# Kernel tuning notes

Measured on AMD Instinct MI355X. Metric: run time of the kernel, lower is better.

## Reference

```python
import jax, jax.numpy as jnp
import numpy as np

TOP_K = 2

def setup_inputs() -> dict:
    key = jax.random.key(0)
    ks = jax.random.split(key, 5)
    B, S, D, E, R, H = 4, 2048, 1024, 8, 128, 4096
    s = 0.02
    return {
        "hidden_states": jax.random.normal(ks[0], (B, S, D), jnp.float32),
        "w_route": jax.random.normal(ks[1], (E, D, R), jnp.float32) * s,
        "w3": jax.random.normal(ks[2], (E, D, H), jnp.float32) * s,
        "wr2h": jax.random.normal(ks[3], (E, R, H), jnp.float32) * s,
        "wh2d": jax.random.normal(ks[4], (E, H, D), jnp.float32) * s,
    }

def reference(hidden_states, w_route, w3, wr2h, wh2d):
    B, S, D = hidden_states.shape
    E = w_route.shape[0]
    x = hidden_states.reshape(-1, D)                      # [N, D]
    N = x.shape[0]
    # per-expert routing activations (also reused as w1_state inside experts)
    acts = jnp.einsum('nd,edr->ner', x, w_route)          # [N, E, R]
    norms = jnp.linalg.norm(acts, axis=-1)                # [N, E] router logits
    probs = jax.nn.softmax(norms.astype(jnp.float32), axis=-1)
    topw, sel = jax.lax.top_k(probs, TOP_K)               # [N, k]
    topw = topw / topw.sum(axis=-1, keepdims=True)
    topw = topw.astype(x.dtype)
    # dense combine weights: routing weight if expert selected, else 0
    combine = jnp.zeros((N, E), x.dtype).at[jnp.arange(N)[:, None], sel].add(topw)
    out = jnp.zeros_like(x)
    for e in range(E):  # fixed small expert count
        h = (x @ w3[e]) * jax.nn.silu(acts[:, e, :] @ wr2h[e])  # [N, H]
        out = out + (h @ wh2d[e]) * combine[:, e:e + 1]
    final = out.reshape(B, S, D)
    # load balancing loss on the router logits (expert_act_norms)
    mask = jax.nn.one_hot(sel, E, dtype=jnp.float32)      # [N, k, E]
    tokens_per_expert = mask.mean(axis=0)                 # [k, E]
    router_prob_per_expert = probs.mean(axis=0)           # [E]
    bl_loss = jnp.sum(tokens_per_expert * router_prob_per_expert[None, :]) * E
    return final, norms, bl_loss
```

## Files before the change

kernel.cpp:

```cpp
#include <hip/hip_runtime.h>


#define DEV static __device__ __forceinline__

typedef float  f32x4  __attribute__((ext_vector_type(4)));
typedef __bf16 bf16x8 __attribute__((ext_vector_type(8)));

#define VMCNT_(n) asm volatile("s_waitcnt vmcnt(" #n ")" ::: "memory")
#define VMCNT(n) VMCNT_(n)

DEV unsigned short f2bf(float f) {
  union { float f; unsigned u; } v; v.f = f;
  unsigned r = v.u + 0x7fffu + ((v.u >> 16) & 1u);
  return (unsigned short)(r >> 16);
}
DEV float bf2f(unsigned short b) {
  union { unsigned u; float f; } v; v.u = ((unsigned)b) << 16;
  return v.f;
}

DEV void gll16(const void* g, void* l) {
  __builtin_amdgcn_global_load_lds(
      (const __attribute__((address_space(1))) unsigned int*)g,
      (__attribute__((address_space(3))) unsigned int*)l, 16, 0, 0);
}

DEV f32x4 mfma16(bf16x8 a, bf16x8 b, f32x4 c) {
  return __builtin_amdgcn_mfma_f32_16x16x32_bf16(a, b, c, 0, 0, 0);
}

DEV int xcd_swz_gen(int bid, int nwg) {
  int x = bid & 7, o = bid >> 3;
  int q = nwg >> 3, r = nwg & 7;
  return (x < r ? x * (q + 1) : r * (q + 1) + (x - r) * q) + o;
}

DEV bf16x8 frag_read(const unsigned short* lds, int row, int kb) {
  int off = row * 128 + ((kb * 2) ^ ((row & 7) << 4));
  return *(const bf16x8*)((const char*)lds + off);
}
DEV void stage_linear(const unsigned short* base, size_t pitch, int k0,
                      unsigned short* lds, int tid) {
  int wq = tid >> 6, lane = tid & 63;
#pragma unroll
  for (int i = 0; i < 4; ++i) {
    int s = wq * 256 + i * 64 + lane;
    int row = s >> 3, b = s & 7;
    int bb = b ^ (row & 7);
    const unsigned short* g = base + (size_t)row * pitch + (size_t)(k0 + bb * 8);
    gll16(g, lds + (size_t)(wq * 256 + i * 64) * 8);
  }
}
DEV void stage_gather(const unsigned short* base, size_t pitch, size_t colOff,
                      int k0, const int* toks, unsigned short* lds, int tid) {
  int wq = tid >> 6, lane = tid & 63;
#pragma unroll
  for (int i = 0; i < 4; ++i) {
    int s = wq * 256 + i * 64 + lane;
    int row = s >> 3, b = s & 7;
    int bb = b ^ (row & 7);
    const unsigned short* g =
        base + (size_t)toks[row] * pitch + colOff + (size_t)(k0 + bb * 8);
    gll16(g, lds + (size_t)(wq * 256 + i * 64) * 8);
  }
}
DEV void mfma_block(const unsigned short* A, const unsigned short* B,
                    f32x4 (&acc)[4][4], int wm, int wn, int lg, int lc) {
#pragma unroll
  for (int ks = 0; ks < 2; ++ks) {
    int kb = ks * 32 + lg * 8;
    bf16x8 af[4], bff[4];
#pragma unroll
    for (int i = 0; i < 4; ++i) {
      af[i]  = frag_read(A, wm * 64 + i * 16 + lc, kb);
      bff[i] = frag_read(B, wn * 64 + i * 16 + lc, kb);
    }
#pragma unroll
    for (int mf = 0; mf < 4; ++mf)
#pragma unroll
      for (int nf = 0; nf < 4; ++nf)
        acc[mf][nf] = mfma16(af[mf], bff[nf], acc[mf][nf]);
  }
}


__global__ __launch_bounds__(256) void k_cast_x(const float* __restrict__ x,
    unsigned short* __restrict__ xh, unsigned short* __restrict__ xl) {
  int stride = gridDim.x * blockDim.x;
  for (int i = blockIdx.x * blockDim.x + threadIdx.x; i < 8192 * 1024 / 4;
       i += stride) {
    float4 v = ((const float4*)x)[i];
    ushort4 h, l;
    h.x = f2bf(v.x); l.x = f2bf(v.x - bf2f(h.x));
    h.y = f2bf(v.y); l.y = f2bf(v.y - bf2f(h.y));
    h.z = f2bf(v.z); l.z = f2bf(v.z - bf2f(h.z));
    h.w = f2bf(v.w); l.w = f2bf(v.w - bf2f(h.w));
    ((ushort4*)xh)[i] = h;
    ((ushort4*)xl)[i] = l;
  }
}

__global__ void k_zero(int* cnt, float* probsum) {
  int t = threadIdx.x;
  if (t < 16) cnt[t] = 0;
  if (t < 8)  probsum[t] = 0.f;
}

__global__ __launch_bounds__(256) void k_transp(const float* __restrict__ src,
    unsigned short* __restrict__ dst, int K, int N) {
  int ntn = N >> 6;
  int kt = blockIdx.x / ntn, nt = blockIdx.x % ntn;
  int e = blockIdx.y;
  __shared__ float tl[64][65];
  const float* s = src + (size_t)e * K * N;
  unsigned short* d = dst + (size_t)e * N * K;
  int tid = threadIdx.x;
  int c4 = (tid & 15) * 4, rr = tid >> 4;
#pragma unroll
  for (int p = 0; p < 4; ++p) {
    int row = rr + p * 16;
    float4 v = *(const float4*)(s + (size_t)(kt * 64 + row) * N + nt * 64 + c4);
    tl[row][c4] = v.x; tl[row][c4 + 1] = v.y;
    tl[row][c4 + 2] = v.z; tl[row][c4 + 3] = v.w;
  }
  __syncthreads();
#pragma unroll
  for (int p = 0; p < 4; ++p) {
    int n = rr + p * 16;
    ushort4 o;
    o.x = f2bf(tl[c4 + 0][n]); o.y = f2bf(tl[c4 + 1][n]);
    o.z = f2bf(tl[c4 + 2][n]); o.w = f2bf(tl[c4 + 3][n]);
    *(ushort4*)(d + (size_t)(nt * 64 + n) * K + kt * 64 + c4) = o;
  }
}

__global__ __launch_bounds__(256) void k_transp_split(const float* __restrict__ src,
    unsigned short* __restrict__ dh, unsigned short* __restrict__ dl, int K, int N) {
  int ntn = N >> 6;
  int kt = blockIdx.x / ntn, nt = blockIdx.x % ntn;
  int e = blockIdx.y;
  __shared__ float tl[64][65];
  const float* s = src + (size_t)e * K * N;
  size_t dbase = (size_t)e * N * K;
  int tid = threadIdx.x;
  int c4 = (tid & 15) * 4, rr = tid >> 4;
#pragma unroll
  for (int p = 0; p < 4; ++p) {
    int row = rr + p * 16;
    float4 v = *(const float4*)(s + (size_t)(kt * 64 + row) * N + nt * 64 + c4);
    tl[row][c4] = v.x; tl[row][c4 + 1] = v.y;
    tl[row][c4 + 2] = v.z; tl[row][c4 + 3] = v.w;
  }
  __syncthreads();
#pragma unroll
  for (int p = 0; p < 4; ++p) {
    int n = rr + p * 16;
    ushort4 oh, ol;
#pragma unroll
    for (int i = 0; i < 4; ++i) {
      float v = tl[c4 + i][n];
      unsigned short hh = f2bf(v);
      unsigned short ll = f2bf(v - bf2f(hh));
      ((unsigned short*)&oh)[i] = hh;
      ((unsigned short*)&ol)[i] = ll;
    }
    *(ushort4*)(dh + dbase + (size_t)(nt * 64 + n) * K + kt * 64 + c4) = oh;
    *(ushort4*)(dl + dbase + (size_t)(nt * 64 + n) * K + kt * 64 + c4) = ol;
  }
}

__global__ __launch_bounds__(256) void k_route_gemm(
    const unsigned short* __restrict__ xh, const unsigned short* __restrict__ xl,
    const unsigned short* __restrict__ wrh_t, const unsigned short* __restrict__ wrl_t,
    unsigned short* __restrict__ acts, float* __restrict__ norms_out) {
  __shared__ __align__(16) unsigned short Ah[128 * 64], Al[128 * 64];
  __shared__ __align__(16) unsigned short Bh[128 * 64], Bl[128 * 64];
  __shared__ float ssq_s[128][2];
  int tid = threadIdx.x;
  int mt = blockIdx.x, e = blockIdx.y;
  int wq = tid >> 6, lane = tid & 63;
  int wm = wq >> 1, wn = wq & 1, lg = lane >> 4, lc = lane & 15;
  f32x4 acc[4][4] = {};
  const unsigned short* ah_src = xh + (size_t)mt * 128 * 1024;
  const unsigned short* al_src = xl + (size_t)mt * 128 * 1024;
  const unsigned short* bh_src = wrh_t + (size_t)e * 128 * 1024;
  const unsigned short* bl_src = wrl_t + (size_t)e * 128 * 1024;
  for (int kt = 0; kt < 16; ++kt) {
    int k0 = kt * 64;
    stage_linear(ah_src, 1024, k0, Ah, tid);
    stage_linear(al_src, 1024, k0, Al, tid);
    stage_linear(bh_src, 1024, k0, Bh, tid);
    stage_linear(bl_src, 1024, k0, Bl, tid);
    __syncthreads();
#pragma unroll
    for (int ks = 0; ks < 2; ++ks) {
      int kb = ks * 32 + lg * 8;
      bf16x8 ahf[4], alf[4], bhf[4], blf[4];
#pragma unroll
      for (int i = 0; i < 4; ++i) {
        ahf[i] = frag_read(Ah, wm * 64 + i * 16 + lc, kb);
        alf[i] = frag_read(Al, wm * 64 + i * 16 + lc, kb);
        bhf[i] = frag_read(Bh, wn * 64 + i * 16 + lc, kb);
        blf[i] = frag_read(Bl, wn * 64 + i * 16 + lc, kb);
      }
#pragma unroll
      for (int mf = 0; mf < 4; ++mf)
#pragma unroll
        for (int nf = 0; nf < 4; ++nf) {
          acc[mf][nf] = mfma16(ahf[mf], bhf[nf], acc[mf][nf]);
          acc[mf][nf] = mfma16(alf[mf], bhf[nf], acc[mf][nf]);
          acc[mf][nf] = mfma16(ahf[mf], blf[nf], acc[mf][nf]);
        }
    }
    __syncthreads();
  }
  float ssq[4][4];
#pragma unroll
  for (int mf = 0; mf < 4; ++mf)
#pragma unroll
    for (int r = 0; r < 4; ++r) ssq[mf][r] = 0.f;
#pragma unroll
  for (int mf = 0; mf < 4; ++mf)
#pragma unroll
    for (int nf = 0; nf < 4; ++nf)
#pragma unroll
      for (int r = 0; r < 4; ++r) {
        float v = acc[mf][nf][r];
        int row = wm * 64 + mf * 16 + lg * 4 + r;
        int col = wn * 64 + nf * 16 + lc;
        acts[(size_t)(mt * 128 + row) * 1024 + e * 128 + col] = f2bf(v);
        ssq[mf][r] += v * v;
      }
#pragma unroll
  for (int mf = 0; mf < 4; ++mf)
#pragma unroll
    for (int r = 0; r < 4; ++r) {
      float s = ssq[mf][r];
      s += __shfl_xor(s, 1); s += __shfl_xor(s, 2);
      s += __shfl_xor(s, 4); s += __shfl_xor(s, 8);
      if (lc == 0) ssq_s[wm * 64 + mf * 16 + lg * 4 + r][wn] = s;
    }
  __syncthreads();
  if (tid < 128) {
    float s = ssq_s[tid][0] + ssq_s[tid][1];
    norms_out[(size_t)(mt * 128 + tid) * 8 + e] = sqrtf(s);
  }
}

__global__ __launch_bounds__(256) void k_router(const float* __restrict__ norms,
    float* __restrict__ topw, int* __restrict__ sel,
    int* __restrict__ cnt, float* __restrict__ probsum) {
  __shared__ float ps_s[8];
  __shared__ int cnt_s[16];
  int tid = threadIdx.x;
  if (tid < 8)  ps_s[tid] = 0.f;
  if (tid < 16) cnt_s[tid] = 0;
  __syncthreads();
  int n = blockIdx.x * 256 + tid;
  float p[8], mx = -3.4e38f;
#pragma unroll
  for (int e = 0; e < 8; ++e) { p[e] = norms[(size_t)n * 8 + e]; mx = fmaxf(mx, p[e]); }
  float s = 0.f;
#pragma unroll
  for (int e = 0; e < 8; ++e) { p[e] = __expf(p[e] - mx); s += p[e]; }
  float inv = 1.f / s;
  int i1 = 0; float v1 = p[0];
#pragma unroll
  for (int e = 1; e < 8; ++e) if (p[e] > v1) { v1 = p[e]; i1 = e; }
  int i2 = -1; float v2 = -1.f;
#pragma unroll
  for (int e = 0; e < 8; ++e) if (e != i1 && p[e] > v2) { v2 = p[e]; i2 = e; }
  float wsum = v1 + v2;
  topw[n * 2 + 0] = v1 / wsum;
  topw[n * 2 + 1] = v2 / wsum;
  sel[n * 2 + 0] = i1;
  sel[n * 2 + 1] = i2;
  atomicAdd(&cnt_s[i1], 1);
  atomicAdd(&cnt_s[8 + i2], 1);
#pragma unroll
  for (int e = 0; e < 8; ++e) atomicAdd(&ps_s[e], p[e] * inv);
  __syncthreads();
  if (tid < 8)  atomicAdd(&probsum[tid], ps_s[tid]);
  if (tid < 16) atomicAdd(&cnt[tid], cnt_s[tid]);
}

__global__ void k_plan(const int* __restrict__ cnt, const float* __restrict__ probsum,
                       int* __restrict__ offs, int* __restrict__ fill,
                       int4* __restrict__ tilemap, float* __restrict__ bl_out) {
  int4* map256 = tilemap;
  int4* map128 = tilemap + 80;
  int t = 0;
  for (int k = 0; k < 2; ++k) {
    int pos = 0;
    for (int e = 0; e < 8; ++e) {
      int c = cnt[k * 8 + e];
      offs[k * 8 + e] = pos;
      int ntl = (c + 255) >> 8;
      for (int i = 0; i < ntl; ++i) {
        int rr = c - i * 256; if (rr > 256) rr = 256;
        map256[t] = make_int4(e, k * 8192 + pos + i * 256, rr, 0);
        ++t;
      }
      pos += c;
    }
  }
  for (; t < 80; ++t) map256[t] = make_int4(0, 0, 0, 0);
  for (int i = 0; i < 80; ++i) {
    int4 m = map256[i];
    for (int h = 0; h < 2; ++h) {
      int r = m.z - h * 128;
      if (r < 0) r = 0; if (r > 128) r = 128;
      map128[i * 2 + h] = make_int4(m.x, m.y + h * 128, r, 0);
    }
  }
  for (int i = 0; i < 16; ++i) fill[i] = 0;
  float bl = 0.f;
  for (int e = 0; e < 8; ++e)
    bl += ((float)(cnt[e] + cnt[8 + e]) / 8192.f) * (probsum[e] / 8192.f);
  *bl_out = bl * 8.f;
}

__global__ __launch_bounds__(256) void k_fill(const int* __restrict__ sel,
    const float* __restrict__ topw, const int* __restrict__ offs,
    int* __restrict__ fill, int* __restrict__ list01, float* __restrict__ wlist) {
  int n = blockIdx.x * 256 + threadIdx.x;
#pragma unroll
  for (int k = 0; k < 2; ++k) {
    int e = sel[n * 2 + k];
    int pos = atomicAdd(&fill[k * 8 + e], 1);
    int idx = k * 8192 + offs[k * 8 + e] + pos;
    list01[idx] = n;
    wlist[idx] = topw[n * 2 + k];
  }
}

__global__ __launch_bounds__(256) void k_gemm1(
    const unsigned short* __restrict__ xh, const unsigned short* __restrict__ acts,
    const unsigned short* __restrict__ w3t, const unsigned short* __restrict__ wr2h_t,
    const int* __restrict__ list, const int4* __restrict__ tilemap, int tile_lo,
    int nt, unsigned short* __restrict__ hbuf) {
  __shared__ __align__(16) unsigned short A[128 * 64], B[128 * 64];
  __shared__ int toks[128];
  int wg = xcd_swz_gen((int)blockIdx.x, nt * 32);
  int tloc = wg >> 5, bn = wg & 31;
  int4 ent = tilemap[tile_lo + tloc];
  int e = ent.x, posbase = ent.y, rows = ent.z;
  if (rows == 0) return;
  int tid = threadIdx.x;
  if (tid < 128) {
    int rr = tid < rows ? tid : rows - 1;
    toks[tid] = list[posbase + rr];
  }
  __syncthreads();
  int wq = tid >> 6, lane = tid & 63;
  int wm = wq >> 1, wn = wq & 1, lg = lane >> 4, lc = lane & 15;
  f32x4 acc_a[4][4] = {};
  const unsigned short* bsrc = w3t + ((size_t)e * 4096 + bn * 128) * 1024;
  for (int kt = 0; kt < 16; ++kt) {
    int k0 = kt * 64;
    stage_gather(xh, 1024, 0, k0, toks, A, tid);
    stage_linear(bsrc, 1024, k0, B, tid);
    __syncthreads();
    mfma_block(A, B, acc_a, wm, wn, lg, lc);
    __syncthreads();
  }
  f32x4 acc_s[4][4] = {};
  const unsigned short* b2src = wr2h_t + ((size_t)e * 4096 + bn * 128) * 128;
  for (int kt = 0; kt < 2; ++kt) {
    int k0 = kt * 64;
    stage_gather(acts, 1024, (size_t)e * 128, k0, toks, A, tid);
    stage_linear(b2src, 128, k0, B, tid);
    __syncthreads();
    mfma_block(A, B, acc_s, wm, wn, lg, lc);
    __syncthreads();
  }
  size_t hrow0 = (size_t)tloc * 128;
#pragma unroll
  for (int mf = 0; mf < 4; ++mf)
#pragma unroll
    for (int nf = 0; nf < 4; ++nf)
#pragma unroll
      for (int r = 0; r < 4; ++r) {
        int row = wm * 64 + mf * 16 + lg * 4 + r;
        if (row < rows) {
          int col = wn * 64 + nf * 16 + lc;
          float sv = acc_s[mf][nf][r];
          float hv = acc_a[mf][nf][r] * (sv / (1.f + __expf(-sv)));
          hbuf[(hrow0 + row) * 4096 + (size_t)bn * 128 + col] = f2bf(hv);
        }
      }
}

__global__ __launch_bounds__(512, 2) void k_gemm2(
    const unsigned short* __restrict__ hbuf, const unsigned short* __restrict__ wh2dt,
    const int* __restrict__ list, const float* __restrict__ wlist,
    const int4* __restrict__ map256, int tile_lo, int nt,
    float* __restrict__ out) {
  __shared__ __align__(16) unsigned short SA[2][256 * 64];
  __shared__ __align__(16) unsigned short SB[2][256 * 64];
  __shared__ int toks[256];
  __shared__ float wr_s[256];
  int wg = xcd_swz_gen((int)blockIdx.x, nt * 8);
  int tloc = wg >> 3, bn = (wg >> 1) & 3, ks = wg & 1;
  int4 ent = map256[tile_lo + tloc];
  int e = ent.x, posbase = ent.y, rows = ent.z;
  if (rows == 0) return;
  int tid = threadIdx.x;
  if (tid < 256) {
    int rr = tid < rows ? tid : rows - 1;
    toks[tid] = list[posbase + rr];
    wr_s[tid] = wlist[posbase + rr];
  }
  __syncthreads();
  int wq = tid >> 6, lane = tid & 63;
  int wm = wq >> 2, wn = wq & 3, lg = lane >> 4, lc = lane & 15;
  int kbase = ks * 2048;

  int s0 = tid, s1 = tid + 512;
  int r0 = s0 >> 3, c0 = ((s0 & 7) ^ (r0 & 7)) * 8;
  int r1 = s1 >> 3, c1 = ((s1 & 7) ^ (r1 & 7)) * 8;
  const unsigned short* a0 = hbuf + ((size_t)tloc * 256 + r0) * 4096 + kbase + c0;
  const unsigned short* a1 = hbuf + ((size_t)tloc * 256 + r1) * 4096 + kbase + c1;
  const unsigned short* b0 =
      wh2dt + ((size_t)e * 1024 + bn * 256 + r0) * 4096 + kbase + c0;
  const unsigned short* b1 =
      wh2dt + ((size_t)e * 1024 + bn * 256 + r1) * 4096 + kbase + c1;

  auto stA = [&](int kt, int h, int bi) {
    size_t ho = (size_t)h * 128 * 4096;
    gll16(a0 + ho + kt * 64, &SA[bi][(size_t)(h * 1024 + s0) * 8]);
    gll16(a1 + ho + kt * 64, &SA[bi][(size_t)(h * 1024 + s1) * 8]);
  };
  auto stB = [&](int kt, int h, int bi) {
    size_t ho = (size_t)h * 128 * 4096;
    gll16(b0 + ho + kt * 64, &SB[bi][(size_t)(h * 1024 + s0) * 8]);
    gll16(b1 + ho + kt * 64, &SB[bi][(size_t)(h * 1024 + s1) * 8]);
  };

  f32x4 acc[2][4][2][2] = {};
  bf16x8 af[4][2], bf[2][2][2];

#define RA(BI, QM)                                                           \
  _Pragma("unroll") for (int mf = 0; mf < 4; ++mf)                           \
  _Pragma("unroll") for (int k2 = 0; k2 < 2; ++k2)                           \
    af[mf][k2] = frag_read(SA[BI], wm * 128 + QM * 64 + mf * 16 + lc,        \
                           k2 * 32 + lg * 8);
#define RB(BI, QN)                                                           \
  _Pragma("unroll") for (int nf = 0; nf < 2; ++nf)                           \
  _Pragma("unroll") for (int k2 = 0; k2 < 2; ++k2)                           \
    bf[QN][nf][k2] = frag_read(SB[BI], wn * 64 + QN * 32 + nf * 16 + lc,     \
                               k2 * 32 + lg * 8);
#define PH_MMA(QM, QN)                                                       \
  __builtin_amdgcn_sched_barrier(0);                                         \
  __builtin_amdgcn_s_barrier();                                              \
  asm volatile("s_waitcnt lgkmcnt(0)" ::: "memory");                         \
  __builtin_amdgcn_sched_barrier(0);                                         \
  __builtin_amdgcn_s_setprio(1);                                             \
  _Pragma("unroll") for (int mf = 0; mf < 4; ++mf)                           \
  _Pragma("unroll") for (int nf = 0; nf < 2; ++nf)                           \
  _Pragma("unroll") for (int k2 = 0; k2 < 2; ++k2)                           \
    acc[QM][mf][QN][nf] =                                                    \
        mfma16(af[mf][k2], bf[QN][nf][k2], acc[QM][mf][QN][nf]);             \
  __builtin_amdgcn_s_setprio(0);                                             \
  __builtin_amdgcn_sched_barrier(0);                                         \
  __builtin_amdgcn_s_barrier();

  stA(0, 0, 0); stA(0, 1, 0); stB(0, 0, 0); stB(0, 1, 0);
  stB(1, 0, 1); stB(1, 1, 1);
  VMCNT(4);
  __builtin_amdgcn_s_barrier();

  for (int it = 0; it < 15; ++it) {
    int u = 2 * it;
    RA(0, 0); RB(0, 0); stA(u + 1, 0, 1);
    PH_MMA(0, 0);
    RB(0, 1); stA(u + 1, 1, 1);
    PH_MMA(0, 1);
    RA(0, 1); stB(u + 2, 0, 0);
    PH_MMA(1, 1);
    stB(u + 2, 1, 0);
    VMCNT(4);
    PH_MMA(1, 0);
    RA(1, 0); RB(1, 0); stA(u + 2, 0, 0);
    PH_MMA(0, 0);
    RB(1, 1); stA(u + 2, 1, 0);
    PH_MMA(0, 1);
    RA(1, 1); stB(u + 3, 0, 1);
    PH_MMA(1, 1);
    stB(u + 3, 1, 1);
    VMCNT(4);
    PH_MMA(1, 0);
  }
  {
    RA(0, 0); RB(0, 0); stA(31, 0, 1);
    PH_MMA(0, 0);
    RB(0, 1); stA(31, 1, 1);
    PH_MMA(0, 1);
    RA(0, 1);
    PH_MMA(1, 1);
    VMCNT(0);
    PH_MMA(1, 0);
    RA(1, 0); RB(1, 0);
    PH_MMA(0, 0);
    RB(1, 1);
    PH_MMA(0, 1);
    RA(1, 1);
    PH_MMA(1, 1);
    PH_MMA(1, 0);
  }
#undef RA
#undef RB
#undef PH_MMA

#pragma unroll
  for (int qm = 0; qm < 2; ++qm)
#pragma unroll
    for (int mf = 0; mf < 4; ++mf)
#pragma unroll
      for (int qn = 0; qn < 2; ++qn)
#pragma unroll
        for (int nf = 0; nf < 2; ++nf)
#pragma unroll
          for (int r = 0; r < 4; ++r) {
            int row = wm * 128 + qm * 64 + mf * 16 + lg * 4 + r;
            if (row < rows) {
              int col = wn * 64 + qn * 32 + nf * 16 + lc;
              float v = acc[qm][mf][qn][nf][r] * wr_s[row];
              atomicAdd(out + (size_t)toks[row] * 1024 + bn * 256 + col, v);
            }
          }
}


extern "C" void kernel_launch(void* const* d_in, const int* in_sizes, int n_in,
                              void* d_out, int out_size, void* d_ws, size_t ws_size,
                              hipStream_t stream) {
  (void)in_sizes; (void)n_in; (void)out_size;
  const float* x      = (const float*)d_in[0];
  const float* wroute = (const float*)d_in[1];
  const float* w3     = (const float*)d_in[2];
  const float* wr2h   = (const float*)d_in[3];
  const float* wh2d   = (const float*)d_in[4];
  float* out = (float*)d_out;

  char* ws = (char*)d_ws;
  size_t off = 0;
  auto carve = [&](size_t bytes) -> void* {
    void* p = ws + off; off += (bytes + 255) & ~(size_t)255; return p;
  };
  unsigned short* xh     = (unsigned short*)carve((size_t)8192 * 1024 * 2);
  unsigned short* xl     = (unsigned short*)carve((size_t)8192 * 1024 * 2);
  unsigned short* wrh_t  = (unsigned short*)carve((size_t)8 * 128 * 1024 * 2);
  unsigned short* wrl_t  = (unsigned short*)carve((size_t)8 * 128 * 1024 * 2);
  unsigned short* w3t    = (unsigned short*)carve((size_t)8 * 4096 * 1024 * 2);
  unsigned short* wr2h_t = (unsigned short*)carve((size_t)8 * 4096 * 128 * 2);
  unsigned short* wh2dt  = (unsigned short*)carve((size_t)8 * 1024 * 4096 * 2);
  unsigned short* acts   = (unsigned short*)carve((size_t)8192 * 1024 * 2);
  int*   list01 = (int*)carve(2 * 8192 * 4);
  float* wlist  = (float*)carve(2 * 8192 * 4);
  int*   sel    = (int*)carve(8192 * 2 * 4);
  float* topw   = (float*)carve(8192 * 2 * 4);
  int*   ctr    = (int*)carve(8192);
  int* cnt = ctr; int* fill = ctr + 16; int* offs = ctr + 32;
  float* probsum = (float*)(ctr + 48);
  int4* tilemap = (int4*)(ctr + 64);

  size_t avail = ws_size > off ? ws_size - off : 0;
  int tpc = 0;
  const int cands[4] = {160, 80, 40, 20};
  for (int i = 0; i < 4; ++i) {
    if ((size_t)cands[i] * 128 * 4096 * 2 <= avail) { tpc = cands[i]; break; }
  }
  if (!tpc) return;
  unsigned short* hbuf = (unsigned short*)(ws + off);

  float* norms_out = out + 8388608;
  float* bl_out    = out + 8454144;

  hipMemsetAsync(out, 0, (size_t)8388608 * 4, stream);
  k_cast_x<<<2048, 256, 0, stream>>>(x, xh, xl);
  k_zero<<<1, 64, 0, stream>>>(cnt, probsum);
  k_transp<<<dim3(16 * 64, 8), 256, 0, stream>>>(w3, w3t, 1024, 4096);
  k_transp<<<dim3(64 * 16, 8), 256, 0, stream>>>(wh2d, wh2dt, 4096, 1024);
  k_transp<<<dim3(2 * 64, 8), 256, 0, stream>>>(wr2h, wr2h_t, 128, 4096);
  k_transp_split<<<dim3(16 * 2, 8), 256, 0, stream>>>(wroute, wrh_t, wrl_t, 1024, 128);
  k_route_gemm<<<dim3(64, 8), 256, 0, stream>>>(xh, xl, wrh_t, wrl_t, acts, norms_out);
  k_router<<<32, 256, 0, stream>>>(norms_out, topw, sel, cnt, probsum);
  k_plan<<<1, 1, 0, stream>>>(cnt, probsum, offs, fill, tilemap, bl_out);
  k_fill<<<32, 256, 0, stream>>>(sel, topw, offs, fill, list01, wlist);

  int nchunk = (160 + tpc - 1) / tpc;
  for (int c = 0; c < nchunk; ++c) {
    int tile_lo = c * tpc;
    int nt = 160 - tile_lo < tpc ? 160 - tile_lo : tpc;
    k_gemm1<<<nt * 32, 256, 0, stream>>>(
        xh, acts, w3t, wr2h_t, list01, tilemap + 80, tile_lo, nt, hbuf);
    k_gemm2<<<(nt / 2) * 8, 512, 0, stream>>>(
        hbuf, wh2dt, list01, wlist, tilemap, tile_lo / 2, nt / 2, out);
  }
}
```

Before: 802.8 us.

## Rewrite expert up-projection GEMM as 256x128 tile with double-buffered 8-wave pipeline

The first expert GEMM (x@w3 gated by silu of acts@wr2h) moves from 128x128 tiles with 4 waves and single-buffered LDS to 256x128 tiles with 8 waves, double-buffered LDS and interleaved global-to-LDS loads for the next k-step during MFMA phases. Both GEMMs now run in one continuous 18-step k-loop with explicit waitcnt and barriers and raised wave priority around the MFMAs. The aim is to hide load latency, improve operand reuse and halve the number of blocks. The cost is heavier LDS and register use, more hand-written scheduling, and a larger wasted fraction on partially filled 256-row tiles.

```diff
diff --git a/kernel.cpp b/kernel.cpp
--- a/kernel.cpp
+++ b/kernel.cpp
@@ -48,19 +48,6 @@
     int row = s >> 3, b = s & 7;
     int bb = b ^ (row & 7);
     const unsigned short* g = base + (size_t)row * pitch + (size_t)(k0 + bb * 8);
-    gll16(g, lds + (size_t)(wq * 256 + i * 64) * 8);
-  }
-}
-DEV void stage_gather(const unsigned short* base, size_t pitch, size_t colOff,
-                      int k0, const int* toks, unsigned short* lds, int tid) {
-  int wq = tid >> 6, lane = tid & 63;
-#pragma unroll
-  for (int i = 0; i < 4; ++i) {
-    int s = wq * 256 + i * 64 + lane;
-    int row = s >> 3, b = s & 7;
-    int bb = b ^ (row & 7);
-    const unsigned short* g =
-        base + (size_t)toks[row] * pitch + colOff + (size_t)(k0 + bb * 8);
     gll16(g, lds + (size_t)(wq * 256 + i * 64) * 8);
   }
 }
@@ -288,7 +275,6 @@
                        int* __restrict__ offs, int* __restrict__ fill,
                        int4* __restrict__ tilemap, float* __restrict__ bl_out) {
   int4* map256 = tilemap;
-  int4* map128 = tilemap + 80;
   int t = 0;
   for (int k = 0; k < 2; ++k) {
     int pos = 0;
@@ -305,14 +291,6 @@
     }
   }
   for (; t < 80; ++t) map256[t] = make_int4(0, 0, 0, 0);
-  for (int i = 0; i < 80; ++i) {
-    int4 m = map256[i];
-    for (int h = 0; h < 2; ++h) {
-      int r = m.z - h * 128;
-      if (r < 0) r = 0; if (r > 128) r = 128;
-      map128[i * 2 + h] = make_int4(m.x, m.y + h * 128, r, 0);
-    }
-  }
   for (int i = 0; i < 16; ++i) fill[i] = 0;
   float bl = 0.f;
   for (int e = 0; e < 8; ++e)
@@ -334,61 +312,147 @@
   }
 }
 
-__global__ __launch_bounds__(256) void k_gemm1(
+__global__ __launch_bounds__(512, 2) void k_gemm1(
     const unsigned short* __restrict__ xh, const unsigned short* __restrict__ acts,
     const unsigned short* __restrict__ w3t, const unsigned short* __restrict__ wr2h_t,
-    const int* __restrict__ list, const int4* __restrict__ tilemap, int tile_lo,
+    const int* __restrict__ list, const int4* __restrict__ map256, int tile_lo,
     int nt, unsigned short* __restrict__ hbuf) {
-  __shared__ __align__(16) unsigned short A[128 * 64], B[128 * 64];
-  __shared__ int toks[128];
+  __shared__ __align__(16) unsigned short SA[2][256 * 64];
+  __shared__ __align__(16) unsigned short SB[2][128 * 64];
+  __shared__ int toks[256];
   int wg = xcd_swz_gen((int)blockIdx.x, nt * 32);
   int tloc = wg >> 5, bn = wg & 31;
-  int4 ent = tilemap[tile_lo + tloc];
+  int4 ent = map256[tile_lo + tloc];
   int e = ent.x, posbase = ent.y, rows = ent.z;
   if (rows == 0) return;
   int tid = threadIdx.x;
-  if (tid < 128) {
+  if (tid < 256) {
     int rr = tid < rows ? tid : rows - 1;
     toks[tid] = list[posbase + rr];
   }
   __syncthreads();
   int wq = tid >> 6, lane = tid & 63;
-  int wm = wq >> 1, wn = wq & 1, lg = lane >> 4, lc = lane & 15;
-  f32x4 acc_a[4][4] = {};
-  const unsigned short* bsrc = w3t + ((size_t)e * 4096 + bn * 128) * 1024;
-  for (int kt = 0; kt < 16; ++kt) {
-    int k0 = kt * 64;
-    stage_gather(xh, 1024, 0, k0, toks, A, tid);
-    stage_linear(bsrc, 1024, k0, B, tid);
-    __syncthreads();
-    mfma_block(A, B, acc_a, wm, wn, lg, lc);
-    __syncthreads();
-  }
-  f32x4 acc_s[4][4] = {};
-  const unsigned short* b2src = wr2h_t + ((size_t)e * 4096 + bn * 128) * 128;
-  for (int kt = 0; kt < 2; ++kt) {
-    int k0 = kt * 64;
-    stage_gather(acts, 1024, (size_t)e * 128, k0, toks, A, tid);
-    stage_linear(b2src, 128, k0, B, tid);
-    __syncthreads();
-    mfma_block(A, B, acc_s, wm, wn, lg, lc);
-    __syncthreads();
-  }
-  size_t hrow0 = (size_t)tloc * 128;
-#pragma unroll
-  for (int mf = 0; mf < 4; ++mf)
-#pragma unroll
-    for (int nf = 0; nf < 4; ++nf)
-#pragma unroll
-      for (int r = 0; r < 4; ++r) {
-        int row = wm * 64 + mf * 16 + lg * 4 + r;
-        if (row < rows) {
-          int col = wn * 64 + nf * 16 + lc;
-          float sv = acc_s[mf][nf][r];
-          float hv = acc_a[mf][nf][r] * (sv / (1.f + __expf(-sv)));
-          hbuf[(hrow0 + row) * 4096 + (size_t)bn * 128 + col] = f2bf(hv);
+  int wm = wq >> 2, wn = wq & 3, lg = lane >> 4, lc = lane & 15;
+
+  int s0 = tid, s1 = tid + 512;
+  int r0 = s0 >> 3, c0 = ((s0 & 7) ^ (r0 & 7)) * 8;
+  int r1 = s1 >> 3, c1 = ((s1 & 7) ^ (r1 & 7)) * 8;
+  const unsigned short* a00 = xh + (size_t)toks[r0] * 1024 + c0;
+  const unsigned short* a01 = xh + (size_t)toks[r1] * 1024 + c1;
+  const unsigned short* a10 = xh + (size_t)toks[128 + r0] * 1024 + c0;
+  const unsigned short* a11 = xh + (size_t)toks[128 + r1] * 1024 + c1;
+  ptrdiff_t dA = (acts - xh) + e * 128;
+  int rb = tid >> 3, cb = ((tid & 7) ^ (rb & 7)) * 8;
+  const unsigned short* b0 = w3t + ((size_t)e * 4096 + bn * 128 + rb) * 1024 + cb;
+  const unsigned short* b1 = w3t + ((size_t)e * 4096 + bn * 128 + 64 + rb) * 1024 + cb;
+  const unsigned short* q0 = wr2h_t + ((size_t)e * 4096 + bn * 128 + rb) * 128 + cb;
+  const unsigned short* q1 = wr2h_t + ((size_t)e * 4096 + bn * 128 + 64 + rb) * 128 + cb;
+
+  auto stA = [&](int kt, int h, int bi) {
+    unsigned short* d0 = &SA[bi][(size_t)(h * 1024 + s0) * 8];
+    unsigned short* d1 = &SA[bi][(size_t)(h * 1024 + s1) * 8];
+    const unsigned short* p0 = h ? a10 : a00;
+    const unsigned short* p1 = h ? a11 : a01;
+    if (kt < 16) { gll16(p0 + kt * 64, d0); gll16(p1 + kt * 64, d1); }
+    else {
+      gll16(p0 + dA + (kt - 16) * 64, d0);
+      gll16(p1 + dA + (kt - 16) * 64, d1);
+    }
+  };
+  auto stB = [&](int kt, int h, int bi) {
+    unsigned short* d = &SB[bi][(size_t)(h * 512 + tid) * 8];
+    if (kt < 16) gll16((h ? b1 : b0) + kt * 64, d);
+    else         gll16((h ? q1 : q0) + (kt - 16) * 64, d);
+  };
+
+  f32x4 acc_a[2][4][2] = {}, acc_g[2][4][2] = {};
+  bf16x8 af[4][2], bf[2][2];
+
+#define RA1(BI, QM)                                                          \
+  _Pragma("unroll") for (int mf = 0; mf < 4; ++mf)                           \
+  _Pragma("unroll") for (int k2 = 0; k2 < 2; ++k2)                           \
+    af[mf][k2] = frag_read(SA[BI], wm * 128 + QM * 64 + mf * 16 + lc,        \
+                           k2 * 32 + lg * 8);
+#define RB1(BI, QN)                                                          \
+  _Pragma("unroll") for (int k2 = 0; k2 < 2; ++k2)                           \
+    bf[QN][k2] = frag_read(SB[BI], wn * 32 + QN * 16 + lc, k2 * 32 + lg * 8);
+#define PH1(ACC, QM, QN)                                                     \
+  __builtin_amdgcn_sched_barrier(0);                                         \
+  __builtin_amdgcn_s_barrier();                                              \
+  asm volatile("s_waitcnt lgkmcnt(0)" ::: "memory");                         \
+  __builtin_amdgcn_sched_barrier(0);                                         \
+  __builtin_amdgcn_s_setprio(1);                                             \
+  _Pragma("unroll") for (int mf = 0; mf < 4; ++mf)                           \
+  _Pragma("unroll") for (int k2 = 0; k2 < 2; ++k2)                           \
+    ACC[QM][mf][QN] = mfma16(af[mf][k2], bf[QN][k2], ACC[QM][mf][QN]);       \
+  __builtin_amdgcn_s_setprio(0);                                             \
+  __builtin_amdgcn_sched_barrier(0);                                         \
+  __builtin_amdgcn_s_barrier();
+
+  stA(0, 0, 0); stA(0, 1, 0); stB(0, 0, 0); stB(0, 1, 0);
+  stB(1, 0, 1); stB(1, 1, 1);
+  VMCNT(2);
+  __builtin_amdgcn_s_barrier();
+
+  for (int it = 0; it < 8; ++it) {
+    int u = 2 * it;
+    RA1(0, 0); RB1(0, 0); stA(u + 1, 0, 1);
+    PH1(acc_a, 0, 0);
+    RB1(0, 1); stA(u + 1, 1, 1);
+    PH1(acc_a, 0, 1);
+    RA1(0, 1); stB(u + 2, 0, 0);
+    PH1(acc_a, 1, 1);
+    stB(u + 2, 1, 0);
+    VMCNT(2);
+    PH1(acc_a, 1, 0);
+    RA1(1, 0); RB1(1, 0); stA(u + 2, 0, 0);
+    PH1(acc_a, 0, 0);
+    RB1(1, 1); stA(u + 2, 1, 0);
+    PH1(acc_a, 0, 1);
+    RA1(1, 1); stB(u + 3, 0, 1);
+    PH1(acc_a, 1, 1);
+    stB(u + 3, 1, 1);
+    VMCNT(2);
+    PH1(acc_a, 1, 0);
+  }
+  {
+    RA1(0, 0); RB1(0, 0); stA(17, 0, 1);
+    PH1(acc_g, 0, 0);
+    RB1(0, 1); stA(17, 1, 1);
+    PH1(acc_g, 0, 1);
+    RA1(0, 1);
+    PH1(acc_g, 1, 1);
+    VMCNT(0);
+    PH1(acc_g, 1, 0);
+    RA1(1, 0); RB1(1, 0);
+    PH1(acc_g, 0, 0);
+    RB1(1, 1);
+    PH1(acc_g, 0, 1);
+    RA1(1, 1);
+    PH1(acc_g, 1, 1);
+    PH1(acc_g, 1, 0);
+  }
+#undef RA1
+#undef RB1
+#undef PH1
+
+  size_t hrow0 = (size_t)tloc * 256;
+#pragma unroll
+  for (int qm = 0; qm < 2; ++qm)
+#pragma unroll
+    for (int mf = 0; mf < 4; ++mf)
+#pragma unroll
+      for (int qn = 0; qn < 2; ++qn)
+#pragma unroll
+        for (int r = 0; r < 4; ++r) {
+          int row = wm * 128 + qm * 64 + mf * 16 + lg * 4 + r;
+          if (row < rows) {
+            int col = wn * 32 + qn * 16 + lc;
+            float sv = acc_g[qm][mf][qn][r];
+            float hv = acc_a[qm][mf][qn][r] * (sv / (1.f + __expf(-sv)));
+            hbuf[(hrow0 + row) * 4096 + (size_t)bn * 128 + col] = f2bf(hv);
+          }
         }
-      }
 }
 
 __global__ __launch_bounds__(512, 2) void k_gemm2(
@@ -593,8 +657,8 @@
   for (int c = 0; c < nchunk; ++c) {
     int tile_lo = c * tpc;
     int nt = 160 - tile_lo < tpc ? 160 - tile_lo : tpc;
-    k_gemm1<<<nt * 32, 256, 0, stream>>>(
-        xh, acts, w3t, wr2h_t, list01, tilemap + 80, tile_lo, nt, hbuf);
+    k_gemm1<<<(nt / 2) * 32, 512, 0, stream>>>(
+        xh, acts, w3t, wr2h_t, list01, tilemap, tile_lo / 2, nt / 2, hbuf);
     k_gemm2<<<(nt / 2) * 8, 512, 0, stream>>>(
         hbuf, wh2dt, list01, wlist, tilemap, tile_lo / 2, nt / 2, out);
   }
```

Result: faster. 784.2 us (-2.3%).

## Split gate GEMM out and run x@w3 with pipelined 256x256 gather kernel

Applied to the files above, without the earlier changes.

Moves the small silu gate GEMM (acts@wr2h) into its own kernel that writes the gate to hbuf. The large x@w3 GEMM now uses the double-buffered 256x256 tile pipeline with direct global-to-LDS gathered token rows, and multiplies the result by the stored gate in its epilogue. The aim is better MFMA utilisation and data reuse on the dominant GEMM than the old 128x128 kernel, which did not overlap loads with compute. The cost is an extra kernel launch and an extra read and write of hbuf per element. The gemm2 block index mapping is also reordered.

```diff
diff --git a/kernel.cpp b/kernel.cpp
--- a/kernel.cpp
+++ b/kernel.cpp
@@ -288,7 +288,6 @@
                        int* __restrict__ offs, int* __restrict__ fill,
                        int4* __restrict__ tilemap, float* __restrict__ bl_out) {
   int4* map256 = tilemap;
-  int4* map128 = tilemap + 80;
   int t = 0;
   for (int k = 0; k < 2; ++k) {
     int pos = 0;
@@ -305,14 +304,6 @@
     }
   }
   for (; t < 80; ++t) map256[t] = make_int4(0, 0, 0, 0);
-  for (int i = 0; i < 80; ++i) {
-    int4 m = map256[i];
-    for (int h = 0; h < 2; ++h) {
-      int r = m.z - h * 128;
-      if (r < 0) r = 0; if (r > 128) r = 128;
-      map128[i * 2 + h] = make_int4(m.x, m.y + h * 128, r, 0);
-    }
-  }
   for (int i = 0; i < 16; ++i) fill[i] = 0;
   float bl = 0.f;
   for (int e = 0; e < 8; ++e)
@@ -334,18 +325,21 @@
   }
 }
 
-__global__ __launch_bounds__(256) void k_gemm1(
-    const unsigned short* __restrict__ xh, const unsigned short* __restrict__ acts,
-    const unsigned short* __restrict__ w3t, const unsigned short* __restrict__ wr2h_t,
-    const int* __restrict__ list, const int4* __restrict__ tilemap, int tile_lo,
-    int nt, unsigned short* __restrict__ hbuf) {
+__global__ __launch_bounds__(256) void k_gate(
+    const unsigned short* __restrict__ acts, const unsigned short* __restrict__ wr2h_t,
+    const int* __restrict__ list, const int4* __restrict__ map256, int tile_lo256,
+    int nt128, unsigned short* __restrict__ hbuf) {
   __shared__ __align__(16) unsigned short A[128 * 64], B[128 * 64];
   __shared__ int toks[128];
-  int wg = xcd_swz_gen((int)blockIdx.x, nt * 32);
-  int tloc = wg >> 5, bn = wg & 31;
-  int4 ent = tilemap[tile_lo + tloc];
-  int e = ent.x, posbase = ent.y, rows = ent.z;
-  if (rows == 0) return;
+  int wg = xcd_swz_gen((int)blockIdx.x, nt128 * 32);
+  int t128 = wg >> 5, bn = wg & 31;
+  int4 ent = map256[tile_lo256 + (t128 >> 1)];
+  int h = t128 & 1;
+  int e = ent.x;
+  int posbase = ent.y + h * 128;
+  int rows = ent.z - h * 128;
+  if (rows <= 0) return;
+  if (rows > 128) rows = 128;
   int tid = threadIdx.x;
   if (tid < 128) {
     int rr = tid < rows ? tid : rows - 1;
@@ -354,27 +348,17 @@
   __syncthreads();
   int wq = tid >> 6, lane = tid & 63;
   int wm = wq >> 1, wn = wq & 1, lg = lane >> 4, lc = lane & 15;
-  f32x4 acc_a[4][4] = {};
-  const unsigned short* bsrc = w3t + ((size_t)e * 4096 + bn * 128) * 1024;
-  for (int kt = 0; kt < 16; ++kt) {
-    int k0 = kt * 64;
-    stage_gather(xh, 1024, 0, k0, toks, A, tid);
-    stage_linear(bsrc, 1024, k0, B, tid);
-    __syncthreads();
-    mfma_block(A, B, acc_a, wm, wn, lg, lc);
-    __syncthreads();
-  }
-  f32x4 acc_s[4][4] = {};
-  const unsigned short* b2src = wr2h_t + ((size_t)e * 4096 + bn * 128) * 128;
+  f32x4 acc[4][4] = {};
+  const unsigned short* bsrc = wr2h_t + ((size_t)e * 4096 + bn * 128) * 128;
   for (int kt = 0; kt < 2; ++kt) {
     int k0 = kt * 64;
     stage_gather(acts, 1024, (size_t)e * 128, k0, toks, A, tid);
-    stage_linear(b2src, 128, k0, B, tid);
+    stage_linear(bsrc, 128, k0, B, tid);
     __syncthreads();
-    mfma_block(A, B, acc_s, wm, wn, lg, lc);
+    mfma_block(A, B, acc, wm, wn, lg, lc);
     __syncthreads();
   }
-  size_t hrow0 = (size_t)tloc * 128;
+  size_t hrow0 = (size_t)t128 * 128;
 #pragma unroll
   for (int mf = 0; mf < 4; ++mf)
 #pragma unroll
@@ -384,24 +368,22 @@
         int row = wm * 64 + mf * 16 + lg * 4 + r;
         if (row < rows) {
           int col = wn * 64 + nf * 16 + lc;
-          float sv = acc_s[mf][nf][r];
-          float hv = acc_a[mf][nf][r] * (sv / (1.f + __expf(-sv)));
-          hbuf[(hrow0 + row) * 4096 + (size_t)bn * 128 + col] = f2bf(hv);
+          float sv = acc[mf][nf][r];
+          float g = sv / (1.f + __expf(-sv));
+          hbuf[(hrow0 + row) * 4096 + (size_t)bn * 128 + col] = f2bf(g);
         }
       }
 }
 
-__global__ __launch_bounds__(512, 2) void k_gemm2(
-    const unsigned short* __restrict__ hbuf, const unsigned short* __restrict__ wh2dt,
-    const int* __restrict__ list, const float* __restrict__ wlist,
-    const int4* __restrict__ map256, int tile_lo, int nt,
-    float* __restrict__ out) {
+__global__ __launch_bounds__(512, 2) void k_gemm1(
+    const unsigned short* __restrict__ xh, const unsigned short* __restrict__ w3t,
+    const int* __restrict__ list, const int4* __restrict__ map256, int tile_lo,
+    int nt, unsigned short* __restrict__ hbuf) {
   __shared__ __align__(16) unsigned short SA[2][256 * 64];
   __shared__ __align__(16) unsigned short SB[2][256 * 64];
   __shared__ int toks[256];
-  __shared__ float wr_s[256];
-  int wg = xcd_swz_gen((int)blockIdx.x, nt * 8);
-  int tloc = wg >> 3, bn = (wg >> 1) & 3, ks = wg & 1;
+  int wg = xcd_swz_gen((int)blockIdx.x, nt * 16);
+  int tloc = wg >> 4, bn = wg & 15;
   int4 ent = map256[tile_lo + tloc];
   int e = ent.x, posbase = ent.y, rows = ent.z;
   if (rows == 0) return;
@@ -409,30 +391,29 @@
   if (tid < 256) {
     int rr = tid < rows ? tid : rows - 1;
     toks[tid] = list[posbase + rr];
-    wr_s[tid] = wlist[posbase + rr];
   }
   __syncthreads();
   int wq = tid >> 6, lane = tid & 63;
   int wm = wq >> 2, wn = wq & 3, lg = lane >> 4, lc = lane & 15;
-  int kbase = ks * 2048;
 
   int s0 = tid, s1 = tid + 512;
   int r0 = s0 >> 3, c0 = ((s0 & 7) ^ (r0 & 7)) * 8;
   int r1 = s1 >> 3, c1 = ((s1 & 7) ^ (r1 & 7)) * 8;
-  const unsigned short* a0 = hbuf + ((size_t)tloc * 256 + r0) * 4096 + kbase + c0;
-  const unsigned short* a1 = hbuf + ((size_t)tloc * 256 + r1) * 4096 + kbase + c1;
-  const unsigned short* b0 =
-      wh2dt + ((size_t)e * 1024 + bn * 256 + r0) * 4096 + kbase + c0;
-  const unsigned short* b1 =
-      wh2dt + ((size_t)e * 1024 + bn * 256 + r1) * 4096 + kbase + c1;
+  const unsigned short* a00 = xh + (size_t)toks[r0] * 1024 + c0;
+  const unsigned short* a01 = xh + (size_t)toks[r1] * 1024 + c1;
+  const unsigned short* a10 = xh + (size_t)toks[128 + r0] * 1024 + c0;
+  const unsigned short* a11 = xh + (size_t)toks[128 + r1] * 1024 + c1;
+  const unsigned short* b0 = w3t + ((size_t)e * 4096 + bn * 256 + r0) * 1024 + c0;
+  const unsigned short* b1 = w3t + ((size_t)e * 4096 + bn * 256 + r1) * 1024 + c1;
 
   auto stA = [&](int kt, int h, int bi) {
-    size_t ho = (size_t)h * 128 * 4096;
-    gll16(a0 + ho + kt * 64, &SA[bi][(size_t)(h * 1024 + s0) * 8]);
-    gll16(a1 + ho + kt * 64, &SA[bi][(size_t)(h * 1024 + s1) * 8]);
+    const unsigned short* p0 = h ? a10 : a00;
+    const unsigned short* p1 = h ? a11 : a01;
+    gll16(p0 + kt * 64, &SA[bi][(size_t)(h * 1024 + s0) * 8]);
+    gll16(p1 + kt * 64, &SA[bi][(size_t)(h * 1024 + s1) * 8]);
   };
   auto stB = [&](int kt, int h, int bi) {
-    size_t ho = (size_t)h * 128 * 4096;
+    size_t ho = (size_t)h * 128 * 1024;
     gll16(b0 + ho + kt * 64, &SB[bi][(size_t)(h * 1024 + s0) * 8]);
     gll16(b1 + ho + kt * 64, &SB[bi][(size_t)(h * 1024 + s1) * 8]);
   };
@@ -470,6 +451,148 @@
   VMCNT(4);
   __builtin_amdgcn_s_barrier();
 
+  for (int it = 0; it < 7; ++it) {
+    int u = 2 * it;
+    RA(0, 0); RB(0, 0); stA(u + 1, 0, 1);
+    PH_MMA(0, 0);
+    RB(0, 1); stA(u + 1, 1, 1);
+    PH_MMA(0, 1);
+    RA(0, 1); stB(u + 2, 0, 0);
+    PH_MMA(1, 1);
+    stB(u + 2, 1, 0);
+    VMCNT(4);
+    PH_MMA(1, 0);
+    RA(1, 0); RB(1, 0); stA(u + 2, 0, 0);
+    PH_MMA(0, 0);
+    RB(1, 1); stA(u + 2, 1, 0);
+    PH_MMA(0, 1);
+    RA(1, 1); stB(u + 3, 0, 1);
+    PH_MMA(1, 1);
+    stB(u + 3, 1, 1);
+    VMCNT(4);
+    PH_MMA(1, 0);
+  }
+  {
+    RA(0, 0); RB(0, 0); stA(15, 0, 1);
+    PH_MMA(0, 0);
+    RB(0, 1); stA(15, 1, 1);
+    PH_MMA(0, 1);
+    RA(0, 1);
+    PH_MMA(1, 1);
+    VMCNT(0);
+    PH_MMA(1, 0);
+    RA(1, 0); RB(1, 0);
+    PH_MMA(0, 0);
+    RB(1, 1);
+    PH_MMA(0, 1);
+    RA(1, 1);
+    PH_MMA(1, 1);
+    PH_MMA(1, 0);
+  }
+#undef RA
+#undef RB
+#undef PH_MMA
+
+  size_t hrow0 = (size_t)tloc * 256;
+#pragma unroll
+  for (int qm = 0; qm < 2; ++qm)
+#pragma unroll
+    for (int mf = 0; mf < 4; ++mf)
+#pragma unroll
+      for (int qn = 0; qn < 2; ++qn)
+#pragma unroll
+        for (int nf = 0; nf < 2; ++nf)
+#pragma unroll
+          for (int r = 0; r < 4; ++r) {
+            int row = wm * 128 + qm * 64 + mf * 16 + lg * 4 + r;
+            if (row < rows) {
+              int col = wn * 64 + qn * 32 + nf * 16 + lc;
+              size_t idx = (hrow0 + row) * 4096 + (size_t)bn * 256 + col;
+              float g = bf2f(hbuf[idx]);
+              hbuf[idx] = f2bf(acc[qm][mf][qn][nf][r] * g);
+            }
+          }
+}
+
+__global__ __launch_bounds__(512, 2) void k_gemm2(
+    const unsigned short* __restrict__ hbuf, const unsigned short* __restrict__ wh2dt,
+    const int* __restrict__ list, const float* __restrict__ wlist,
+    const int4* __restrict__ map256, int tile_lo, int nt,
+    float* __restrict__ out) {
+  __shared__ __align__(16) unsigned short SA[2][256 * 64];
+  __shared__ __align__(16) unsigned short SB[2][256 * 64];
+  __shared__ int toks[256];
+  __shared__ float wr_s[256];
+  int wg = xcd_swz_gen((int)blockIdx.x, nt * 8);
+  int tloc = wg >> 3, bn = wg & 3, ks = (wg >> 2) & 1;
+  int4 ent = map256[tile_lo + tloc];
+  int e = ent.x, posbase = ent.y, rows = ent.z;
+  if (rows == 0) return;
+  int tid = threadIdx.x;
+  if (tid < 256) {
+    int rr = tid < rows ? tid : rows - 1;
+    toks[tid] = list[posbase + rr];
+    wr_s[tid] = wlist[posbase + rr];
+  }
+  __syncthreads();
+  int wq = tid >> 6, lane = tid & 63;
+  int wm = wq >> 2, wn = wq & 3, lg = lane >> 4, lc = lane & 15;
+  int kbase = ks * 2048;
+
+  int s0 = tid, s1 = tid + 512;
+  int r0 = s0 >> 3, c0 = ((s0 & 7) ^ (r0 & 7)) * 8;
+  int r1 = s1 >> 3, c1 = ((s1 & 7) ^ (r1 & 7)) * 8;
+  const unsigned short* a0 = hbuf + ((size_t)tloc * 256 + r0) * 4096 + kbase + c0;
+  const unsigned short* a1 = hbuf + ((size_t)tloc * 256 + r1) * 4096 + kbase + c1;
+  const unsigned short* b0 =
+      wh2dt + ((size_t)e * 1024 + bn * 256 + r0) * 4096 + kbase + c0;
+  const unsigned short* b1 =
+      wh2dt + ((size_t)e * 1024 + bn * 256 + r1) * 4096 + kbase + c1;
+
+  auto stA = [&](int kt, int h, int bi) {
+    size_t ho = (size_t)h * 128 * 4096;
+    gll16(a0 + ho + kt * 64, &SA[bi][(size_t)(h * 1024 + s0) * 8]);
+    gll16(a1 + ho + kt * 64, &SA[bi][(size_t)(h * 1024 + s1) * 8]);
+  };
+  auto stB = [&](int kt, int h, int bi) {
+    size_t ho = (size_t)h * 128 * 4096;
+    gll16(b0 + ho + kt * 64, &SB[bi][(size_t)(h * 1024 + s0) * 8]);
+    gll16(b1 + ho + kt * 64, &SB[bi][(size_t)(h * 1024 + s1) * 8]);
+  };
+
+  f32x4 acc[2][4][2][2] = {};
+  bf16x8 af[4][2], bf[2][2][2];
+
+#define RA(BI, QM)                                                           \
+  _Pragma("unroll") for (int mf = 0; mf < 4; ++mf)                           \
+  _Pragma("unroll") for (int k2 = 0; k2 < 2; ++k2)                           \
+    af[mf][k2] = frag_read(SA[BI], wm * 128 + QM * 64 + mf * 16 + lc,        \
+                           k2 * 32 + lg * 8);
+#define RB(BI, QN)                                                           \
+  _Pragma("unroll") for (int nf = 0; nf < 2; ++nf)                           \
+  _Pragma("unroll") for (int k2 = 0; k2 < 2; ++k2)                           \
+    bf[QN][nf][k2] = frag_read(SB[BI], wn * 64 + QN * 32 + nf * 16 + lc,     \
+                               k2 * 32 + lg * 8);
+#define PH_MMA(QM, QN)                                                       \
+  __builtin_amdgcn_sched_barrier(0);                                         \
+  __builtin_amdgcn_s_barrier();                                              \
+  asm volatile("s_waitcnt lgkmcnt(0)" ::: "memory");                         \
+  __builtin_amdgcn_sched_barrier(0);                                         \
+  __builtin_amdgcn_s_setprio(1);                                             \
+  _Pragma("unroll") for (int mf = 0; mf < 4; ++mf)                           \
+  _Pragma("unroll") for (int nf = 0; nf < 2; ++nf)                           \
+  _Pragma("unroll") for (int k2 = 0; k2 < 2; ++k2)                           \
+    acc[QM][mf][QN][nf] =                                                    \
+        mfma16(af[mf][k2], bf[QN][nf][k2], acc[QM][mf][QN][nf]);             \
+  __builtin_amdgcn_s_setprio(0);                                             \
+  __builtin_amdgcn_sched_barrier(0);                                         \
+  __builtin_amdgcn_s_barrier();
+
+  stA(0, 0, 0); stA(0, 1, 0); stB(0, 0, 0); stB(0, 1, 0);
+  stB(1, 0, 1); stB(1, 1, 1);
+  VMCNT(4);
+  __builtin_amdgcn_s_barrier();
+
   for (int it = 0; it < 15; ++it) {
     int u = 2 * it;
     RA(0, 0); RB(0, 0); stA(u + 1, 0, 1);
@@ -593,8 +716,10 @@
   for (int c = 0; c < nchunk; ++c) {
     int tile_lo = c * tpc;
     int nt = 160 - tile_lo < tpc ? 160 - tile_lo : tpc;
-    k_gemm1<<<nt * 32, 256, 0, stream>>>(
-        xh, acts, w3t, wr2h_t, list01, tilemap + 80, tile_lo, nt, hbuf);
+    k_gate<<<nt * 32, 256, 0, stream>>>(
+        acts, wr2h_t, list01, tilemap, tile_lo / 2, nt, hbuf);
+    k_gemm1<<<(nt / 2) * 16, 512, 0, stream>>>(
+        xh, w3t, list01, tilemap, tile_lo / 2, nt / 2, hbuf);
     k_gemm2<<<(nt / 2) * 8, 512, 0, stream>>>(
         hbuf, wh2dt, list01, wlist, tilemap, tile_lo / 2, nt / 2, out);
   }
```

After: 845.5 us. +5.3%, slower.
